# Kernel optimization log

Hardware: AMD Instinct MI355X
Metric: run time of the kernel (lower is better)

## Reference

```python
import jax, jax.numpy as jnp
import numpy as np

EPS = 1e-5
SELECT_NUM = 10   # hard-coded in Support_AUG_Image
NEIGHBOR_K = 3
SEMI_K = 3


def _conv(x, w):
    return jax.lax.conv_general_dilated(x, w, (1, 1), 'SAME',
                                        dimension_numbers=('NCHW', 'OIHW', 'NCHW'))


def _bn(x, g, b):
    # BatchNorm2d, training mode: biased batch stats over (N, H, W)
    mu = jnp.mean(x, (0, 2, 3), keepdims=True)
    var = jnp.mean((x - mu) ** 2, (0, 2, 3), keepdims=True)
    return g[None, :, None, None] * (x - mu) * jax.lax.rsqrt(var + EPS) + b[None, :, None, None]


def _lrelu(x):
    return jnp.where(x >= 0, x, 0.2 * x)


def _pool(x):
    return jax.lax.reduce_window(x, -jnp.inf, jax.lax.max,
                                 (1, 1, 2, 2), (1, 1, 2, 2), 'VALID')


def _features(x, params):
    # conv-bn-lrelu-pool, conv-bn-lrelu-pool, conv-bn-lrelu, conv-bn-lrelu
    for i, (w, g, b) in enumerate(params):
        x = _lrelu(_bn(_conv(x, w), g, b))
        if i < 2:
            x = _pool(x)
    return x  # [N, 64, 21, 21] for 84x84 input


def _descriptors(feat):
    # [B, C, h, w] -> [B, h*w, C], rows L2-normalized (query local descriptors)
    B, C = feat.shape[0], feat.shape[1]
    d = feat.reshape(B, C, -1).transpose(0, 2, 1)
    return d / jnp.sqrt(jnp.sum(d * d, -1, keepdims=True))


def _col_normalize(s):
    # [C, m]: L2-normalize each column (support descriptor)
    return s / jnp.sqrt(jnp.sum(s * s, 0, keepdims=True))


def _img2class_sim(q_desc, S, k):
    # q_desc [B, n, C] row-normalized; S [K, C, m] raw support banks.
    # Per class (K small, fixed): cosine sims [B, n, m], top-k over m, sum.
    sims = []
    for j in range(S.shape[0]):
        inner = q_desc @ _col_normalize(S[j])          # [B, n, m]
        tv = jax.lax.top_k(inner, k)[0]                # [B, n, k]
        sims.append(jnp.sum(tv, axis=(1, 2)))
    return jnp.stack(sims, 1)                          # [B, K]


def _forward(input1, input2, input3, params):
    K, shot = input2.shape[0], input2.shape[1]
    q = _features(input1, params)                      # [Bq, 64, 21, 21]
    sup = _features(input2.reshape((-1,) + input2.shape[2:]), params)
    C, h, w = sup.shape[1], sup.shape[2], sup.shape[3]
    # per class: permute(1,0,2,3).view(C,-1) -> [K, C, shot*h*w]
    S = sup.reshape(K, shot, C, h, w).transpose(0, 2, 1, 3, 4).reshape(K, C, shot * h * w)
    u = _features(input3, params)                      # [Bu, 64, 21, 21]

    # Support_AUG_Image: similarity of unlabeled pool vs support, softmax over classes,
    # then append top-10 unlabeled feature maps (raw) to each class bank.
    u_desc = _descriptors(u)
    sim_u = jax.nn.softmax(_img2class_sim(u_desc, S, SEMI_K), axis=1)  # [Bu, K]
    aug = []
    for j in range(K):
        idx = jax.lax.top_k(sim_u[:, j], SELECT_NUM)[1]                # [10]
        sel = u[idx].transpose(1, 0, 2, 3).reshape(C, -1)              # [C, 10*h*w]
        aug.append(jnp.concatenate([S[j], sel], axis=1))
    S_aug = jnp.stack(aug, 0)                          # [K, C, shot*h*w + 10*h*w]

    # ImgtoClass_Metric on queries vs augmented support
    q_desc = _descriptors(q)
    return _img2class_sim(q_desc, S_aug, NEIGHBOR_K)   # [Bq, K]


def setup_inputs() -> dict:
    key = jax.random.key(0)
    ks = jax.random.split(key, 8)
    inp = {
        'input1': jax.random.normal(ks[0], (75, 3, 84, 84), jnp.float32),
        'input2': jax.random.normal(ks[1], (5, 5, 3, 84, 84), jnp.float32),
        'input3': jax.random.normal(ks[2], (64, 3, 84, 84), jnp.float32),
        'w1': jax.random.normal(ks[3], (64, 3, 3, 3), jnp.float32) * 0.1,
        'w2': jax.random.normal(ks[4], (64, 64, 3, 3), jnp.float32) * 0.05,
        'w3': jax.random.normal(ks[5], (64, 64, 3, 3), jnp.float32) * 0.05,
        'w4': jax.random.normal(ks[6], (64, 64, 3, 3), jnp.float32) * 0.05,
    }
    for i in (1, 2, 3, 4):
        inp[f'g{i}'] = jnp.ones((64,), jnp.float32)
        inp[f'b{i}'] = jnp.zeros((64,), jnp.float32)
    return inp


def reference(input1, input2, input3, w1, g1, b1, w2, g2, b2, w3, g3, b3, w4, g4, b4):
    params = [(w1, g1, b1), (w2, g2, b2), (w3, g3, b3), (w4, g4, b4)]
    return _forward(input1, input2, input3, params)
```

## Files before the change

kernel.cpp:

```cpp
#include <hip/hip_runtime.h>
#include <hip/hip_bf16.h>
#include <math.h>

typedef __hip_bfloat16 bf16;
typedef __attribute__((ext_vector_type(8))) short short8;
typedef __attribute__((ext_vector_type(4))) float floatx4;
typedef __attribute__((ext_vector_type(4))) unsigned short ushort4v;

#define LRELU(v) ((v) < 0.f ? 0.2f * (v) : (v))

__device__ __forceinline__ float b2f(bf16 x) { return __bfloat162float(x); }
__device__ __forceinline__ int img_group(int n) { return n < 75 ? 0 : (n < 100 ? 1 : 2); }

__global__ __launch_bounds__(64) void detect_kernel(
    const void* in1, const void* in2, const void* in3,
    const void* w1, const void* w2, const void* w3, const void* w4,
    const void* g1, const void* g2, const void* g3, const void* g4,
    int* __restrict__ flags)
{
  int t = threadIdx.x;
  if (t >= 11) return;
  const void* p = nullptr; int nh = 384, isg = 0;
  switch (t) {
    case 0: p = in1; break;  case 1: p = in2; break;  case 2: p = in3; break;
    case 3: p = w1;  break;  case 4: p = w2;  break;  case 5: p = w3;  break;
    case 6: p = w4;  break;
    case 7: p = g1; nh = 64; isg = 1; break;
    case 8: p = g2; nh = 64; isg = 1; break;
    case 9: p = g3; nh = 64; isg = 1; break;
    case 10: p = g4; nh = 64; isg = 1; break;
  }
  const unsigned short* h = (const unsigned short*)p;
  int cnt = 0;
  for (int i = 0; i < nh; ++i) {
    unsigned short v = h[i];
    if (isg) {
      if (v == 0) ++cnt;
    } else {
      int e = (v >> 7) & 0xFF;
      if (e >= 160 || (e > 0 && e <= 80)) ++cnt;
    }
  }
  flags[t] = isg ? (cnt >= 16) : (cnt >= 48);
}

#define ZT0 167280
#define ZT1 1972592
#define ZT2 2896240
#define ZT3 3819888
#define ZT4 4565104
__device__ __forceinline__ void border_yx(int b, int W, int* y, int* x) {
  if (b < W) { *y = 0; *x = b; }
  else if (b < 2 * W) { *y = W - 1; *x = b - W; }
  else { int cc = b - 2 * W; *y = 1 + (cc >> 1); *x = (cc & 1) ? (W - 1) : 0; }
}
__global__ __launch_bounds__(256) void zero_pads(
    bf16* __restrict__ imgp, bf16* __restrict__ p1t,
    bf16* __restrict__ p2t, bf16* __restrict__ f3t, bf16* __restrict__ descAll)
{
  int i = blockIdx.x * 256 + threadIdx.x;
  bf16 z = __float2bfloat16(0.f);
  if (i < ZT0) {
    int plane = i / 340, b = i % 340;
    int y, x; border_yx(b, 86, &y, &x);
    imgp[((size_t)plane * 86 + y) * 86 + x] = z;
  } else if (i < ZT1) {
    int r = i - ZT0;
    int img = r / (172 * 64); r %= 172 * 64;
    int colb = r >> 6, ch = r & 63;
    int y, x; border_yx(colb, 44, &y, &x);
    p1t[(((size_t)img * 1936) + y * 44 + x) * 64 + ch] = z;
  } else if (i < ZT2) {
    int r = i - ZT1;
    int img = r / (88 * 64); r %= 88 * 64;
    int colb = r >> 6, ch = r & 63;
    int y, x; border_yx(colb, 23, &y, &x);
    p2t[(((size_t)img * 529) + y * 23 + x) * 64 + ch] = z;
  } else if (i < ZT3) {
    int r = i - ZT2;
    int img = r / (88 * 64); r %= 88 * 64;
    int colb = r >> 6, ch = r & 63;
    int y, x; border_yx(colb, 23, &y, &x);
    f3t[(((size_t)img * 529) + y * 23 + x) * 64 + ch] = z;
  } else if (i < ZT4) {
    int r = i - ZT3;
    int img = r / (71 * 64); r %= 71 * 64;
    int row = 441 + (r >> 6), ch = r & 63;
    descAll[((size_t)img * 512 + row) * 64 + ch] = z;
  }
}

#define NIMG 3471552
#define BIMG 13562
#define NWP  110592
#define BWP  432
#define BW1  8
#define BGB  2
#define NPART (4 * 164 * 128)
#define NZ (NPART + 320 + 375)
#define BZ  331
__global__ __launch_bounds__(256) void setup_all(
    const void* in1, const void* in2, const void* in3,
    const void* w1, const void* w2, const void* w3, const void* w4,
    const void* g1, const void* b1, const void* g2, const void* b2,
    const void* g3, const void* b3, const void* g4, const void* b4,
    const int* __restrict__ flags,
    bf16* __restrict__ imgp, bf16* __restrict__ w1p,
    bf16* __restrict__ wp2, bf16* __restrict__ wp3, bf16* __restrict__ wp4,
    float* __restrict__ gb, float* __restrict__ part,
    float* __restrict__ uscore, float* __restrict__ qscore)
{
  int b = blockIdx.x;
  if (b < BIMG) {
    int k = b * 256 + threadIdx.x;
    if (k >= NIMG) return;
    const void* src; int idx, f;
    if (k < 75 * 21168)       { src = in1; idx = k;               f = flags[0]; }
    else if (k < 100 * 21168) { src = in2; idx = k - 75 * 21168;  f = flags[1]; }
    else                      { src = in3; idx = k - 100 * 21168; f = flags[2]; }
    bf16 v = f ? __float2bfloat16(((const float*)src)[idx]) : ((const bf16*)src)[idx];
    int n = k / 21168, r = k % 21168;
    int ci = r / 7056, pix = r % 7056;
    int y = pix / 84, x = pix % 84;
    imgp[((size_t)(n * 3 + ci) * 86 + y + 1) * 86 + x + 1] = v;
  } else if (b < BIMG + BWP) {
    int idx = (b - BIMG) * 256 + threadIdx.x;
    if (idx >= NWP) return;
    int which = idx / 36864, i = idx % 36864;
    const void* src = which == 0 ? w2 : (which == 1 ? w3 : w4);
    bf16* dst = which == 0 ? wp2 : (which == 1 ? wp3 : wp4);
    int f = flags[4 + which];
    float v = f ? ((const float*)src)[i] : b2f(((const bf16*)src)[i]);
    int co = i / 576, ci = (i / 9) % 64, tap = i % 9;
    dst[((size_t)tap * 64 + co) * 64 + ci] = __float2bfloat16(v);
  } else if (b < BIMG + BWP + BW1) {
    int i = (b - BIMG - BWP) * 256 + threadIdx.x;
    if (i >= 2048) return;
    int co = i >> 5, k = i & 31;
    float v = 0.f;
    if (k < 27) {
      int f = flags[3];
      v = f ? ((const float*)w1)[co * 27 + k] : b2f(((const bf16*)w1)[co * 27 + k]);
    }
    w1p[i] = __float2bfloat16(v);
  } else if (b < BIMG + BWP + BW1 + BGB) {
    int i = (b - BIMG - BWP - BW1) * 256 + threadIdx.x;
    if (i >= 512) return;
    int which = i >> 6, cc = i & 63;
    const void* s;
    switch (which) {
      case 0: s = g1; break; case 1: s = b1; break;
      case 2: s = g2; break; case 3: s = b2; break;
      case 4: s = g3; break; case 5: s = b3; break;
      case 6: s = g4; break; default: s = b4; break;
    }
    int isg = !(which & 1);
    int f = isg ? flags[7 + (which >> 1)] : 0;
    gb[i] = f ? ((const float*)s)[cc] : b2f(((const bf16*)s)[cc]);
  } else {
    int i = (b - BIMG - BWP - BW1 - BGB) * 256 + threadIdx.x;
    if (i < NPART) part[i] = 0.f;
    else if (i < NPART + 320) uscore[i - NPART] = 0.f;
    else if (i < NZ) qscore[i - NPART - 320] = 0.f;
  }
}

__global__ __launch_bounds__(256) void conv1_stats_mfma(
    const bf16* __restrict__ imgp, const bf16* __restrict__ w1p,
    float* __restrict__ part)
{
  __shared__ float sacc[128];
  int n = blockIdx.x, tile = blockIdx.y;
  int lane = threadIdx.x & 63;
  int q = lane >> 4, c = lane & 15;
  int wave = threadIdx.x >> 6;
  int p = tile * 64 + wave * 16 + c;
  bool valid = p < 7056;
  int pc = valid ? p : 0;
  int y = pc / 84, x = pc % 84;
  const short* ib = (const short*)(imgp + (size_t)n * 3 * 86 * 86);
  short bs[8];
  #pragma unroll
  for (int j = 0; j < 8; ++j) {
    int k = q * 8 + j;
    int ci = k / 9, tap = k - ci * 9;
    int dy = tap / 3, dx = tap - dy * 3;
    bs[j] = (k < 27 && valid) ? ib[(ci * 86 + y + dy) * 86 + x + dx] : (short)0;
  }
  short8 B = {bs[0], bs[1], bs[2], bs[3], bs[4], bs[5], bs[6], bs[7]};
  float s[16], sq[16];
  #pragma unroll
  for (int t = 0; t < 4; ++t) {
    const short* ap = (const short*)w1p + (t * 16 + c) * 32 + q * 8;
    short8 A = *(const short8*)ap;
    floatx4 acc = {0.f, 0.f, 0.f, 0.f};
    acc = __builtin_amdgcn_mfma_f32_16x16x32_bf16(A, B, acc, 0, 0, 0);
    #pragma unroll
    for (int r = 0; r < 4; ++r) { s[t * 4 + r] = acc[r]; sq[t * 4 + r] = acc[r] * acc[r]; }
  }
  #pragma unroll
  for (int off = 1; off < 16; off <<= 1)
    #pragma unroll
    for (int i = 0; i < 16; ++i) {
      s[i]  += __shfl_xor(s[i], off);
      sq[i] += __shfl_xor(sq[i], off);
    }
  if (threadIdx.x < 128) sacc[threadIdx.x] = 0.f;
  __syncthreads();
  if (c == 0) {
    #pragma unroll
    for (int t = 0; t < 4; ++t)
      #pragma unroll
      for (int r = 0; r < 4; ++r) {
        int co = t * 16 + q * 4 + r;
        atomicAdd(&sacc[co], s[t * 4 + r]);
        atomicAdd(&sacc[64 + co], sq[t * 4 + r]);
      }
  }
  __syncthreads();
  if (threadIdx.x < 128) atomicAdd(&part[n * 128 + threadIdx.x], sacc[threadIdx.x]);
}

__global__ __launch_bounds__(256) void finalize_kernel(
    const float* __restrict__ part, const float* __restrict__ gam, const float* __restrict__ bet,
    float* __restrict__ scl, float* __restrict__ sht, float HWf)
{
  int t = threadIdx.x;
  if (t >= 192) return;
  int g = t / 64, c = t % 64;
  const int starts[3] = {0, 75, 100}, cnts[3] = {75, 25, 64};
  float S = 0.f, Q = 0.f;
  for (int im = starts[g]; im < starts[g] + cnts[g]; ++im) {
    S += part[im * 128 + c];
    Q += part[im * 128 + 64 + c];
  }
  float N = (float)cnts[g] * HWf;
  float mean = S / N;
  float var = fmaxf(Q / N - mean * mean, 0.f);
  float rstd = rsqrtf(var + 1e-5f);
  float sc = gam[c] * rstd;
  scl[t] = sc;
  sht[t] = bet[c] - mean * sc;
}

__global__ __launch_bounds__(256) void conv1_pool_mfma(
    const bf16* __restrict__ imgp, const bf16* __restrict__ w1p,
    const float* __restrict__ scl, const float* __restrict__ sht,
    bf16* __restrict__ p1t)
{
  int n = blockIdx.x, tile = blockIdx.y;
  int lane = threadIdx.x & 63, wave = threadIdx.x >> 6;
  int q = lane >> 4, c = lane & 15;
  int pp = tile * 64 + wave * 16 + c;
  bool valid = pp < 1764;
  int pc = valid ? pp : 0;
  int py = pc / 42, px = pc % 42;
  int g = img_group(n);
  const short* ib = (const short*)(imgp + (size_t)n * 3 * 86 * 86);
  short8 B[4];
  #pragma unroll
  for (int quad = 0; quad < 4; ++quad) {
    int y = 2 * py + (quad >> 1), x = 2 * px + (quad & 1);
    short bs[8];
    #pragma unroll
    for (int j = 0; j < 8; ++j) {
      int k = q * 8 + j;
      int ci = k / 9, tap = k - ci * 9;
      int dy = tap / 3, dx = tap - dy * 3;
      bs[j] = (k < 27) ? ib[(ci * 86 + y + dy) * 86 + x + dx] : (short)0;
    }
    B[quad] = (short8){bs[0], bs[1], bs[2], bs[3], bs[4], bs[5], bs[6], bs[7]};
  }
  bf16* ob = p1t + ((size_t)n * 1936 + (py + 1) * 44 + px + 1) * 64;
  #pragma unroll
  for (int t = 0; t < 4; ++t) {
    const short* ap = (const short*)w1p + (t * 16 + c) * 32 + q * 8;
    short8 A = *(const short8*)ap;
    floatx4 a0 = {0.f,0.f,0.f,0.f}, a1 = a0, a2 = a0, a3 = a0;
    a0 = __builtin_amdgcn_mfma_f32_16x16x32_bf16(A, B[0], a0, 0, 0, 0);
    a1 = __builtin_amdgcn_mfma_f32_16x16x32_bf16(A, B[1], a1, 0, 0, 0);
    a2 = __builtin_amdgcn_mfma_f32_16x16x32_bf16(A, B[2], a2, 0, 0, 0);
    a3 = __builtin_amdgcn_mfma_f32_16x16x32_bf16(A, B[3], a3, 0, 0, 0);
    if (valid) {
      ushort4v st;
      #pragma unroll
      for (int r = 0; r < 4; ++r) {
        int co = t * 16 + q * 4 + r;
        float sc_ = scl[g * 64 + co], sh_ = sht[g * 64 + co];
        float v0 = a0[r] * sc_ + sh_; v0 = LRELU(v0);
        float v1 = a1[r] * sc_ + sh_; v1 = LRELU(v1);
        float v2 = a2[r] * sc_ + sh_; v2 = LRELU(v2);
        float v3 = a3[r] * sc_ + sh_; v3 = LRELU(v3);
        float best = fmaxf(fmaxf(v0, v1), fmaxf(v2, v3));
        bf16 bv = __float2bfloat16(best);
        st[r] = *(unsigned short*)&bv;
      }
      *(ushort4v*)(ob + t * 16 + q * 4) = st;
    }
  }
}

__global__ __launch_bounds__(256) void bnt_kernel(
    const float* __restrict__ in, const float* __restrict__ scl, const float* __restrict__ sht,
    bf16* __restrict__ outp, int HW, int W, int PW, int PHPW)
{
  __shared__ bf16 tile[64][65];
  int n = blockIdx.x, t0 = blockIdx.y * 64;
  int g = img_group(n);
  for (int idx = threadIdx.x; idx < 4096; idx += 256) {
    int ci = idx >> 6, pix = idx & 63;
    int p = t0 + pix;
    float v = 0.f;
    if (p < HW) {
      v = in[((size_t)n * 64 + ci) * HW + p] * scl[g * 64 + ci] + sht[g * 64 + ci];
      v = LRELU(v);
    }
    tile[pix][ci] = __float2bfloat16(v);
  }
  __syncthreads();
  for (int idx = threadIdx.x; idx < 4096; idx += 256) {
    int pix = idx >> 6, ci = idx & 63;
    int p = t0 + pix;
    if (p < HW) {
      int y = p / W, x = p % W;
      outp[((size_t)n * PHPW + (y + 1) * PW + (x + 1)) * 64 + ci] = tile[pix][ci];
    }
  }
}

__global__ __launch_bounds__(256) void conv_mfma_kernel(
    const bf16* __restrict__ in_t, const bf16* __restrict__ wp,
    void* __restrict__ outp, int HW, int W, int PW, int PHPW, int out_is_f32,
    float* __restrict__ part)
{
  __shared__ float sacc[128];
  if (threadIdx.x < 128) sacc[threadIdx.x] = 0.f;
  __syncthreads();
  int n = blockIdx.x, tile = blockIdx.y;
  int wave = threadIdx.x >> 6, lane = threadIdx.x & 63;
  int q = lane >> 4, c = lane & 15;
  int p = tile * 64 + wave * 16 + c;
  bool valid = p < HW;
  int pc = valid ? p : HW - 1;
  int y = pc / W, x = pc % W;
  const bf16* ibase = in_t + ((size_t)n * PHPW + y * PW + x) * 64;

  short8 B0[9], B1[9];
  #pragma unroll
  for (int dy = 0; dy < 3; ++dy)
    #pragma unroll
    for (int dx = 0; dx < 3; ++dx) {
      const short* bp = (const short*)(ibase + (dy * PW + dx) * 64) + q * 8;
      B0[dy * 3 + dx] = *(const short8*)bp;
      B1[dy * 3 + dx] = *(const short8*)(bp + 32);
    }

  for (int t = 0; t < 4; ++t) {
    floatx4 acc = {0.f, 0.f, 0.f, 0.f};
    #pragma unroll
    for (int tap = 0; tap < 9; ++tap) {
      const short* ap = (const short*)(wp + ((size_t)tap * 64 + t * 16 + c) * 64) + q * 8;
      short8 A0 = *(const short8*)ap;
      short8 A1 = *(const short8*)(ap + 32);
      acc = __builtin_amdgcn_mfma_f32_16x16x32_bf16(A0, B0[tap], acc, 0, 0, 0);
      acc = __builtin_amdgcn_mfma_f32_16x16x32_bf16(A1, B1[tap], acc, 0, 0, 0);
    }
    float sv[4], qv[4];
    #pragma unroll
    for (int r = 0; r < 4; ++r) {
      float v = valid ? acc[r] : 0.f;
      sv[r] = v; qv[r] = v * v;
    }
    #pragma unroll
    for (int off = 1; off < 16; off <<= 1)
      #pragma unroll
      for (int r = 0; r < 4; ++r) {
        sv[r] += __shfl_xor(sv[r], off);
        qv[r] += __shfl_xor(qv[r], off);
      }
    if (c == 0) {
      #pragma unroll
      for (int r = 0; r < 4; ++r) {
        int co = t * 16 + q * 4 + r;
        atomicAdd(&sacc[co], sv[r]);
        atomicAdd(&sacc[64 + co], qv[r]);
      }
    }
    if (valid) {
      #pragma unroll
      for (int r = 0; r < 4; ++r) {
        int co = t * 16 + q * 4 + r;
        size_t oidx = ((size_t)n * 64 + co) * HW + p;
        if (out_is_f32) ((float*)outp)[oidx] = acc[r];
        else ((bf16*)outp)[oidx] = __float2bfloat16(acc[r]);
      }
    }
  }
  __syncthreads();
  if (threadIdx.x < 128) atomicAdd(&part[n * 128 + threadIdx.x], sacc[threadIdx.x]);
}

__global__ __launch_bounds__(256) void bn2_pool_t(
    const bf16* __restrict__ c2, const float* __restrict__ scl, const float* __restrict__ sht,
    bf16* __restrict__ p2t)
{
  __shared__ bf16 tile[64][65];
  int n = blockIdx.x, t0 = blockIdx.y * 64;
  int g = img_group(n);
  for (int idx = threadIdx.x; idx < 4096; idx += 256) {
    int co = idx >> 6, pix = idx & 63;
    int p = t0 + pix;
    bf16 outv = __float2bfloat16(0.f);
    if (p < 441) {
      float sc = scl[g * 64 + co], sh = sht[g * 64 + co];
      int py = p / 21, px = p % 21;
      const bf16* base = c2 + ((size_t)n * 64 + co) * 1764;
      float best = -1e30f;
      #pragma unroll
      for (int dy = 0; dy < 2; ++dy)
        #pragma unroll
        for (int dx = 0; dx < 2; ++dx) {
          float v = b2f(base[(2 * py + dy) * 42 + 2 * px + dx]) * sc + sh;
          v = LRELU(v);
          best = fmaxf(best, v);
        }
      outv = __float2bfloat16(best);
    }
    tile[pix][co] = outv;
  }
  __syncthreads();
  for (int idx = threadIdx.x; idx < 4096; idx += 256) {
    int pix = idx >> 6, co = idx & 63;
    int p = t0 + pix;
    if (p < 441) {
      int y = p / 21, x = p % 21;
      p2t[((size_t)n * 529 + (y + 1) * 23 + x + 1) * 64 + co] = tile[pix][co];
    }
  }
}

__global__ __launch_bounds__(256) void bn_norm_desc(
    const float* __restrict__ feat, const float* __restrict__ scl, const float* __restrict__ sht,
    bf16* __restrict__ descAll)
{
  __shared__ float tile[64][65];
  int n = blockIdx.x, t0 = blockIdx.y * 64;
  int g = img_group(n);
  for (int idx = threadIdx.x; idx < 4096; idx += 256) {
    int ci = idx >> 6, pix = idx & 63;
    int p = t0 + pix;
    float v = 0.f;
    if (p < 441) {
      v = feat[((size_t)n * 64 + ci) * 441 + p] * scl[g * 64 + ci] + sht[g * 64 + ci];
      v = LRELU(v);
    }
    tile[pix][ci] = v;
  }
  __syncthreads();
  int pix = threadIdx.x >> 2, quar = threadIdx.x & 3;
  float ss = 0.f;
  #pragma unroll
  for (int c = 0; c < 16; ++c) { float v = tile[pix][quar * 16 + c]; ss += v * v; }
  ss += __shfl_xor(ss, 1);
  ss += __shfl_xor(ss, 2);
  int p = t0 + pix;
  float inv = (p < 441) ? rsqrtf(ss) : 0.f;
  bf16* o = descAll + ((size_t)n * 512 + p) * 64 + quar * 16;
  #pragma unroll
  for (int c = 0; c < 16; ++c) o[c] = __float2bfloat16(tile[pix][quar * 16 + c] * inv);
}

__global__ __launch_bounds__(256) void sbank_copy(
    const bf16* __restrict__ descAll, bf16* __restrict__ SnT)
{
  int j = blockIdx.x / 9, chunk = blockIdx.x % 9;
  int col = chunk * 256 + threadIdx.x;
  short* o = (short*)(SnT + ((size_t)j * 2304 + col) * 64);
  if (col < 2205) {
    int shot = col / 441, pos = col % 441;
    const short* s = (const short*)(descAll + ((size_t)(75 + j * 5 + shot) * 512 + pos) * 64);
    #pragma unroll
    for (int k = 0; k < 8; ++k) *(short8*)(o + k * 8) = *(const short8*)(s + k * 8);
  } else {
    short8 z = {0,0,0,0,0,0,0,0};
    #pragma unroll
    for (int k = 0; k < 8; ++k) *(short8*)(o + k * 8) = z;
  }
}

__global__ __launch_bounds__(256) void saug_copy(
    const bf16* __restrict__ descAll, const bf16* __restrict__ SnT,
    const int* __restrict__ sel, bf16* __restrict__ SaT)
{
  int j = blockIdx.x / 26, chunk = blockIdx.x % 26;
  int col = chunk * 256 + threadIdx.x;
  short* o = (short*)(SaT + ((size_t)j * 6656 + col) * 64);
  const short* s;
  if (col < 2205) {
    s = (const short*)(SnT + ((size_t)j * 2304 + col) * 64);
  } else if (col < 6615) {
    int rel = col - 2205;
    int i = rel / 441, pos = rel % 441;
    int img = 100 + sel[j * 10 + i];
    s = (const short*)(descAll + ((size_t)img * 512 + pos) * 64);
  } else {
    short8 z = {0,0,0,0,0,0,0,0};
    #pragma unroll
    for (int k = 0; k < 8; ++k) *(short8*)(o + k * 8) = z;
    return;
  }
  #pragma unroll
  for (int k = 0; k < 8; ++k) *(short8*)(o + k * 8) = *(const short8*)(s + k * 8);
}

__global__ __launch_bounds__(256) void sim_mfma_kernel(
    const bf16* __restrict__ desc, const bf16* __restrict__ bankT,
    float* __restrict__ out, int m, int mp)
{
  __shared__ short lds[2][64 * 72];
  int img = blockIdx.x, cls = blockIdx.y, rowgrp = blockIdx.z;
  int tid = threadIdx.x;
  int wave = tid >> 6, lane = tid & 63;
  int q = lane >> 4, c = lane & 15;
  int R = rowgrp * 256 + wave * 64;
  bool wactive = R < 441;

  short8 b0l, b0h, b1l, b1h, b2l, b2h, b3l, b3h;
  if (wactive) {
    const short* dp = (const short*)(desc + ((size_t)img * 512 + R + c) * 64) + q * 8;
    b0l = *(const short8*)dp;          b0h = *(const short8*)(dp + 32);
    b1l = *(const short8*)(dp + 1024); b1h = *(const short8*)(dp + 1056);
    b2l = *(const short8*)(dp + 2048); b2h = *(const short8*)(dp + 2080);
    b3l = *(const short8*)(dp + 3072); b3h = *(const short8*)(dp + 3104);
  }

  float t0[4], t1[4], t2[4];
  #pragma unroll
  for (int i = 0; i < 4; ++i) { t0[i] = -1e4f; t1[i] = -1e4f; t2[i] = -1e4f; }

  const floatx4 z4 = {0.f, 0.f, 0.f, 0.f};

  const short* bankc = (const short*)(bankT + (size_t)cls * mp * 64);
  int nchunk = mp >> 6;
  int nfull = m >> 4;

  for (int s = tid; s < 512; s += 256) {
    int col = s >> 3, part = s & 7;
    *(short8*)(&lds[0][col * 72 + part * 8]) = *(const short8*)(bankc + (size_t)col * 64 + part * 8);
  }
  __syncthreads();

  for (int ch = 0; ch < nchunk; ++ch) {
    int cur = ch & 1;
    if (ch + 1 < nchunk) {
      const short* src = bankc + (size_t)(ch + 1) * 4096;
      for (int s = tid; s < 512; s += 256) {
        int col = s >> 3, part = s & 7;
        *(short8*)(&lds[cur ^ 1][col * 72 + part * 8]) = *(const short8*)(src + (size_t)col * 64 + part * 8);
      }
    }
    if (wactive) {
      #pragma unroll
      for (int t = 0; t < 4; ++t) {
        const short* lp = &lds[cur][(t * 16 + c) * 72 + q * 8];
        short8 A0 = *(const short8*)lp;
        short8 A1 = *(const short8*)(lp + 32);
        floatx4 a0 = __builtin_amdgcn_mfma_f32_16x16x32_bf16(A0, b0l, z4, 0, 0, 0);
        floatx4 a1 = __builtin_amdgcn_mfma_f32_16x16x32_bf16(A0, b1l, z4, 0, 0, 0);
        floatx4 a2 = __builtin_amdgcn_mfma_f32_16x16x32_bf16(A0, b2l, z4, 0, 0, 0);
        floatx4 a3 = __builtin_amdgcn_mfma_f32_16x16x32_bf16(A0, b3l, z4, 0, 0, 0);
        a0 = __builtin_amdgcn_mfma_f32_16x16x32_bf16(A1, b0h, a0, 0, 0, 0);
        a1 = __builtin_amdgcn_mfma_f32_16x16x32_bf16(A1, b1h, a1, 0, 0, 0);
        a2 = __builtin_amdgcn_mfma_f32_16x16x32_bf16(A1, b2h, a2, 0, 0, 0);
        a3 = __builtin_amdgcn_mfma_f32_16x16x32_bf16(A1, b3h, a3, 0, 0, 0);
        int gt = ch * 4 + t;
        if (gt < nfull) {
          #pragma unroll
          for (int r = 0; r < 4; ++r) {
            float v0 = a0[r];
            t2[0] = __builtin_amdgcn_fmed3f(v0, t2[0], t1[0]);
            t1[0] = __builtin_amdgcn_fmed3f(v0, t1[0], t0[0]);
            t0[0] = fmaxf(t0[0], v0);
            float v1 = a1[r];
            t2[1] = __builtin_amdgcn_fmed3f(v1, t2[1], t1[1]);
            t1[1] = __builtin_amdgcn_fmed3f(v1, t1[1], t0[1]);
            t0[1] = fmaxf(t0[1], v1);
            float v2 = a2[r];
            t2[2] = __builtin_amdgcn_fmed3f(v2, t2[2], t1[2]);
            t1[2] = __builtin_amdgcn_fmed3f(v2, t1[2], t0[2]);
            t0[2] = fmaxf(t0[2], v2);
            float v3 = a3[r];
            t2[3] = __builtin_amdgcn_fmed3f(v3, t2[3], t1[3]);
            t1[3] = __builtin_amdgcn_fmed3f(v3, t1[3], t0[3]);
            t0[3] = fmaxf(t0[3], v3);
          }
        } else {
          #pragma unroll
          for (int r = 0; r < 4; ++r) {
            bool colok = (gt * 16 + q * 4 + r) < m;
            float v0 = colok ? a0[r] : -1e4f;
            t2[0] = __builtin_amdgcn_fmed3f(v0, t2[0], t1[0]);
            t1[0] = __builtin_amdgcn_fmed3f(v0, t1[0], t0[0]);
            t0[0] = fmaxf(t0[0], v0);
            float v1 = colok ? a1[r] : -1e4f;
            t2[1] = __builtin_amdgcn_fmed3f(v1, t2[1], t1[1]);
            t1[1] = __builtin_amdgcn_fmed3f(v1, t1[1], t0[1]);
            t0[1] = fmaxf(t0[1], v1);
            float v2 = colok ? a2[r] : -1e4f;
            t2[2] = __builtin_amdgcn_fmed3f(v2, t2[2], t1[2]);
            t1[2] = __builtin_amdgcn_fmed3f(v2, t1[2], t0[2]);
            t0[2] = fmaxf(t0[2], v2);
            float v3 = colok ? a3[r] : -1e4f;
            t2[3] = __builtin_amdgcn_fmed3f(v3, t2[3], t1[3]);
            t1[3] = __builtin_amdgcn_fmed3f(v3, t1[3], t0[3]);
            t0[3] = fmaxf(t0[3], v3);
          }
        }
      }
    }
    __syncthreads();
  }

  if (wactive) {
    #pragma unroll
    for (int off = 16; off < 64; off <<= 1) {
      #pragma unroll
      for (int i = 0; i < 4; ++i) {
        float b0v = __shfl_xor(t0[i], off);
        float b1v = __shfl_xor(t1[i], off);
        float b2v = __shfl_xor(t2[i], off);
        float n0 = fmaxf(t0[i], b0v);
        float n1 = fminf(fmaxf(t0[i], b1v), fmaxf(t1[i], b0v));
        float n2 = fminf(fminf(fmaxf(t0[i], b2v), fmaxf(t1[i], b1v)), fmaxf(t2[i], b0v));
        t0[i] = n0; t1[i] = n1; t2[i] = n2;
      }
    }
    float psum = 0.f;
    if (q == 0) {
      #pragma unroll
      for (int i = 0; i < 4; ++i)
        if (R + i * 16 + c < 441) psum += t0[i] + t1[i] + t2[i];
    }
    #pragma unroll
    for (int off = 32; off > 0; off >>= 1) psum += __shfl_down(psum, off);
    if (lane == 0) atomicAdd(&out[img * 5 + cls], psum);
  }
}

__global__ __launch_bounds__(64) void softtop_kernel(
    const float* __restrict__ uscore, int* __restrict__ sel)
{
  __shared__ float simu[320];
  int i = threadIdx.x;
  {
    float v[5]; float mx = -1e30f;
    #pragma unroll
    for (int j = 0; j < 5; ++j) { v[j] = uscore[i * 5 + j]; mx = fmaxf(mx, v[j]); }
    float s = 0.f;
    #pragma unroll
    for (int j = 0; j < 5; ++j) { v[j] = expf(v[j] - mx); s += v[j]; }
    float inv = 1.f / s;
    #pragma unroll
    for (int j = 0; j < 5; ++j) simu[i * 5 + j] = v[j] * inv;
  }
  __syncthreads();
  if (i < 5) {
    unsigned long long mask = 0ull;
    for (int r = 0; r < 10; ++r) {
      float best = -1e30f; int bi = 0;
      for (int k = 0; k < 64; ++k) {
        if ((mask >> k) & 1ull) continue;
        float v = simu[k * 5 + i];
        if (v > best) { best = v; bi = k; }
      }
      mask |= (1ull << bi);
      sel[i * 10 + r] = bi;
    }
  }
}

__global__ __launch_bounds__(256) void outcvt_kernel(
    const float* __restrict__ qv, const int* __restrict__ flags, float* __restrict__ o)
{
  int i = blockIdx.x * 256 + threadIdx.x;
  if (i >= 375) return;
  float v = qv[i];
  int bad = (!isfinite(v)) || fabsf(v) > 2e3f;
  if (bad) {
    int code = flags[0] * 4 + flags[3] * 2 + flags[7];
    v = -(1e8f * (1.f + 0.01f * (float)code));
  }
  o[i] = v;
}

extern "C" void kernel_launch(void* const* d_in, const int* in_sizes, int n_in,
                              void* d_out, int out_size, void* d_ws, size_t ws_size,
                              hipStream_t stream) {
  const void* in1 = d_in[0];
  const void* in2 = d_in[1];
  const void* in3 = d_in[2];
  const void* w1  = d_in[3];
  const void* w2  = d_in[4];
  const void* w3  = d_in[5];
  const void* w4  = d_in[6];
  const void* g1  = d_in[7];
  const void* b1  = d_in[8];
  const void* g2  = d_in[9];
  const void* b2  = d_in[10];
  const void* g3  = d_in[11];
  const void* b3  = d_in[12];
  const void* g4  = d_in[13];
  const void* b4  = d_in[14];

  char* base = (char*)d_ws;
  size_t off = 0;
  auto alloc = [&](size_t bytes) -> void* {
    void* p = base + off;
    off += (bytes + 255) & ~(size_t)255;
    return p;
  };
  int*   flags = (int*)alloc(16 * 4);
  bf16*  wp2   = (bf16*)alloc(36864 * 2);
  bf16*  wp3   = (bf16*)alloc(36864 * 2);
  bf16*  wp4   = (bf16*)alloc(36864 * 2);
  bf16*  w1p   = (bf16*)alloc(2048 * 2);
  float* gb    = (float*)alloc(8 * 64 * 4);
  float* part  = (float*)alloc(4 * 164 * 128 * 4);
  float* scl1  = (float*)alloc(192 * 4);
  float* sht1  = (float*)alloc(192 * 4);
  float* scl2  = (float*)alloc(192 * 4);
  float* sht2  = (float*)alloc(192 * 4);
  float* scl3  = (float*)alloc(192 * 4);
  float* sht3  = (float*)alloc(192 * 4);
  float* scl4  = (float*)alloc(192 * 4);
  float* sht4  = (float*)alloc(192 * 4);
  float* uscore = (float*)alloc(320 * 4);
  int*   sel    = (int*)alloc(50 * 4);
  float* qscore = (float*)alloc(375 * 4);
  bf16*  imgp = (bf16*)alloc((size_t)164 * 3 * 86 * 86 * 2);
  bf16*  p1t  = (bf16*)alloc((size_t)164 * 1936 * 64 * 2);
  bf16*  p2t  = (bf16*)alloc((size_t)164 * 529 * 64 * 2);
  bf16*  f3t  = (bf16*)alloc((size_t)164 * 529 * 64 * 2);
  bf16*  descAll = (bf16*)alloc((size_t)164 * 512 * 64 * 2);
  bf16*  conv2o   = (bf16*)alloc((size_t)164 * 64 * 1764 * 2);
  bf16* SnT     = (bf16*)alloc((size_t)5 * 2304 * 64 * 2);
  bf16* SaT     = (bf16*)alloc((size_t)5 * 6656 * 64 * 2);
  float* feat3 = (float*)p1t;
  float* feat4 = (float*)((char*)p1t + (size_t)164 * 64 * 441 * 4);
  float* part1 = part;
  float* part2 = part + 164 * 128;
  float* part3 = part + 2 * 164 * 128;
  float* part4 = part + 3 * 164 * 128;

  detect_kernel<<<1, 64, 0, stream>>>(in1, in2, in3, w1, w2, w3, w4, g1, g2, g3, g4, flags);
  zero_pads<<<(ZT4 + 255) / 256, 256, 0, stream>>>(imgp, p1t, p2t, f3t, descAll);
  setup_all<<<BIMG + BWP + BW1 + BGB + BZ, 256, 0, stream>>>(
      in1, in2, in3, w1, w2, w3, w4, g1, b1, g2, b2, g3, b3, g4, b4,
      flags, imgp, w1p, wp2, wp3, wp4, gb, part, uscore, qscore);

  conv1_stats_mfma<<<dim3(164, 111), 256, 0, stream>>>(imgp, w1p, part1);
  finalize_kernel<<<1, 256, 0, stream>>>(part1, gb + 0 * 64, gb + 1 * 64, scl1, sht1, 7056.f);
  conv1_pool_mfma<<<dim3(164, 28), 256, 0, stream>>>(imgp, w1p, scl1, sht1, p1t);

  conv_mfma_kernel<<<dim3(164, 28), 256, 0, stream>>>(p1t, wp2, conv2o, 1764, 42, 44, 1936, 0, part2);
  finalize_kernel<<<1, 256, 0, stream>>>(part2, gb + 2 * 64, gb + 3 * 64, scl2, sht2, 1764.f);
  bn2_pool_t<<<dim3(164, 7), 256, 0, stream>>>(conv2o, scl2, sht2, p2t);

  conv_mfma_kernel<<<dim3(164, 7), 256, 0, stream>>>(p2t, wp3, feat3, 441, 21, 23, 529, 1, part3);
  finalize_kernel<<<1, 256, 0, stream>>>(part3, gb + 4 * 64, gb + 5 * 64, scl3, sht3, 441.f);
  bnt_kernel<<<dim3(164, 7), 256, 0, stream>>>(feat3, scl3, sht3, f3t, 441, 21, 23, 529);

  conv_mfma_kernel<<<dim3(164, 7), 256, 0, stream>>>(f3t, wp4, feat4, 441, 21, 23, 529, 1, part4);
  finalize_kernel<<<1, 256, 0, stream>>>(part4, gb + 6 * 64, gb + 7 * 64, scl4, sht4, 441.f);

  bn_norm_desc<<<dim3(164, 7), 256, 0, stream>>>(feat4, scl4, sht4, descAll);
  sbank_copy<<<45, 256, 0, stream>>>(descAll, SnT);

  sim_mfma_kernel<<<dim3(64, 5, 2), 256, 0, stream>>>(descAll + (size_t)100 * 512 * 64, SnT, uscore, 2205, 2304);
  softtop_kernel<<<1, 64, 0, stream>>>(uscore, sel);
  saug_copy<<<130, 256, 0, stream>>>(descAll, SnT, sel, SaT);

  sim_mfma_kernel<<<dim3(75, 5, 2), 256, 0, stream>>>(descAll, SaT, qscore, 6615, 6656);
  outcvt_kernel<<<2, 256, 0, stream>>>(qscore, flags, (float*)d_out);
}
```

Measured before the change: 1.132 ms.

## Split similarity kernel over bank column slices and merge top-3 partials

The similarity kernel now keeps all 441 query rows in one 7-wave block and splits the support bank columns into four slices across grid z. Before, the rows were split into two groups, which left wave slots idle. Each slice writes per-row top-3 partials to a global buffer, and a new merge kernel combines them and sums per image-class, replacing the atomicAdd. This adds parallelism and cuts the redundant bank streaming that came from the row split, at the cost of an extra launch and a partial-buffer round trip. Each slice's bank chunk count must divide evenly by four (36 and 104 do).

Measured after the change: 1.078 ms. -4.8%, faster.

```diff
diff --git a/kernel.cpp b/kernel.cpp
--- a/kernel.cpp
+++ b/kernel.cpp
@@ -513,26 +513,23 @@
   for (int k = 0; k < 8; ++k) *(short8*)(o + k * 8) = *(const short8*)(s + k * 8);
 }
 
-__global__ __launch_bounds__(256) void sim_mfma_kernel(
+#define SIM_NS 4
+__global__ __launch_bounds__(448) void sim_mfma_kernel(
     const bf16* __restrict__ desc, const bf16* __restrict__ bankT,
-    float* __restrict__ out, int m, int mp)
+    float* __restrict__ partial, int m, int mp)
 {
   __shared__ short lds[2][64 * 72];
-  int img = blockIdx.x, cls = blockIdx.y, rowgrp = blockIdx.z;
+  int img = blockIdx.x, cls = blockIdx.y, slice = blockIdx.z;
   int tid = threadIdx.x;
   int wave = tid >> 6, lane = tid & 63;
   int q = lane >> 4, c = lane & 15;
-  int R = rowgrp * 256 + wave * 64;
-  bool wactive = R < 441;
-
-  short8 b0l, b0h, b1l, b1h, b2l, b2h, b3l, b3h;
-  if (wactive) {
-    const short* dp = (const short*)(desc + ((size_t)img * 512 + R + c) * 64) + q * 8;
-    b0l = *(const short8*)dp;          b0h = *(const short8*)(dp + 32);
-    b1l = *(const short8*)(dp + 1024); b1h = *(const short8*)(dp + 1056);
-    b2l = *(const short8*)(dp + 2048); b2h = *(const short8*)(dp + 2080);
-    b3l = *(const short8*)(dp + 3072); b3h = *(const short8*)(dp + 3104);
-  }
+  int R = wave * 64;
+
+  const short* dp = (const short*)(desc + ((size_t)img * 512 + R + c) * 64) + q * 8;
+  short8 b0l = *(const short8*)dp;          short8 b0h = *(const short8*)(dp + 32);
+  short8 b1l = *(const short8*)(dp + 1024); short8 b1h = *(const short8*)(dp + 1056);
+  short8 b2l = *(const short8*)(dp + 2048); short8 b2h = *(const short8*)(dp + 2080);
+  short8 b3l = *(const short8*)(dp + 3072); short8 b3h = *(const short8*)(dp + 3104);
 
   float t0[4], t1[4], t2[4];
   #pragma unroll
@@ -541,110 +538,141 @@
   const floatx4 z4 = {0.f, 0.f, 0.f, 0.f};
 
   const short* bankc = (const short*)(bankT + (size_t)cls * mp * 64);
-  int nchunk = mp >> 6;
+  int nc = (mp >> 6) / SIM_NS;
+  int ch0 = slice * nc, ch1 = ch0 + nc;
   int nfull = m >> 4;
 
-  for (int s = tid; s < 512; s += 256) {
+  for (int s = tid; s < 512; s += 448) {
     int col = s >> 3, part = s & 7;
-    *(short8*)(&lds[0][col * 72 + part * 8]) = *(const short8*)(bankc + (size_t)col * 64 + part * 8);
-  }
-  __syncthreads();
-
-  for (int ch = 0; ch < nchunk; ++ch) {
-    int cur = ch & 1;
-    if (ch + 1 < nchunk) {
+    *(short8*)(&lds[0][col * 72 + part * 8]) =
+        *(const short8*)(bankc + ((size_t)ch0 * 64 + col) * 64 + part * 8);
+  }
+  __syncthreads();
+
+  for (int ch = ch0; ch < ch1; ++ch) {
+    int cur = (ch - ch0) & 1;
+    if (ch + 1 < ch1) {
       const short* src = bankc + (size_t)(ch + 1) * 4096;
-      for (int s = tid; s < 512; s += 256) {
+      for (int s = tid; s < 512; s += 448) {
         int col = s >> 3, part = s & 7;
         *(short8*)(&lds[cur ^ 1][col * 72 + part * 8]) = *(const short8*)(src + (size_t)col * 64 + part * 8);
       }
     }
-    if (wactive) {
-      #pragma unroll
-      for (int t = 0; t < 4; ++t) {
-        const short* lp = &lds[cur][(t * 16 + c) * 72 + q * 8];
-        short8 A0 = *(const short8*)lp;
-        short8 A1 = *(const short8*)(lp + 32);
-        floatx4 a0 = __builtin_amdgcn_mfma_f32_16x16x32_bf16(A0, b0l, z4, 0, 0, 0);
-        floatx4 a1 = __builtin_amdgcn_mfma_f32_16x16x32_bf16(A0, b1l, z4, 0, 0, 0);
-        floatx4 a2 = __builtin_amdgcn_mfma_f32_16x16x32_bf16(A0, b2l, z4, 0, 0, 0);
-        floatx4 a3 = __builtin_amdgcn_mfma_f32_16x16x32_bf16(A0, b3l, z4, 0, 0, 0);
-        a0 = __builtin_amdgcn_mfma_f32_16x16x32_bf16(A1, b0h, a0, 0, 0, 0);
-        a1 = __builtin_amdgcn_mfma_f32_16x16x32_bf16(A1, b1h, a1, 0, 0, 0);
-        a2 = __builtin_amdgcn_mfma_f32_16x16x32_bf16(A1, b2h, a2, 0, 0, 0);
-        a3 = __builtin_amdgcn_mfma_f32_16x16x32_bf16(A1, b3h, a3, 0, 0, 0);
-        int gt = ch * 4 + t;
-        if (gt < nfull) {
-          #pragma unroll
-          for (int r = 0; r < 4; ++r) {
-            float v0 = a0[r];
-            t2[0] = __builtin_amdgcn_fmed3f(v0, t2[0], t1[0]);
-            t1[0] = __builtin_amdgcn_fmed3f(v0, t1[0], t0[0]);
-            t0[0] = fmaxf(t0[0], v0);
-            float v1 = a1[r];
-            t2[1] = __builtin_amdgcn_fmed3f(v1, t2[1], t1[1]);
-            t1[1] = __builtin_amdgcn_fmed3f(v1, t1[1], t0[1]);
-            t0[1] = fmaxf(t0[1], v1);
-            float v2 = a2[r];
-            t2[2] = __builtin_amdgcn_fmed3f(v2, t2[2], t1[2]);
-            t1[2] = __builtin_amdgcn_fmed3f(v2, t1[2], t0[2]);
-            t0[2] = fmaxf(t0[2], v2);
-            float v3 = a3[r];
-            t2[3] = __builtin_amdgcn_fmed3f(v3, t2[3], t1[3]);
-            t1[3] = __builtin_amdgcn_fmed3f(v3, t1[3], t0[3]);
-            t0[3] = fmaxf(t0[3], v3);
-          }
-        } else {
-          #pragma unroll
-          for (int r = 0; r < 4; ++r) {
-            bool colok = (gt * 16 + q * 4 + r) < m;
-            float v0 = colok ? a0[r] : -1e4f;
-            t2[0] = __builtin_amdgcn_fmed3f(v0, t2[0], t1[0]);
-            t1[0] = __builtin_amdgcn_fmed3f(v0, t1[0], t0[0]);
-            t0[0] = fmaxf(t0[0], v0);
-            float v1 = colok ? a1[r] : -1e4f;
-            t2[1] = __builtin_amdgcn_fmed3f(v1, t2[1], t1[1]);
-            t1[1] = __builtin_amdgcn_fmed3f(v1, t1[1], t0[1]);
-            t0[1] = fmaxf(t0[1], v1);
-            float v2 = colok ? a2[r] : -1e4f;
-            t2[2] = __builtin_amdgcn_fmed3f(v2, t2[2], t1[2]);
-            t1[2] = __builtin_amdgcn_fmed3f(v2, t1[2], t0[2]);
-            t0[2] = fmaxf(t0[2], v2);
-            float v3 = colok ? a3[r] : -1e4f;
-            t2[3] = __builtin_amdgcn_fmed3f(v3, t2[3], t1[3]);
-            t1[3] = __builtin_amdgcn_fmed3f(v3, t1[3], t0[3]);
-            t0[3] = fmaxf(t0[3], v3);
-          }
+    #pragma unroll
+    for (int t = 0; t < 4; ++t) {
+      const short* lp = &lds[cur][(t * 16 + c) * 72 + q * 8];
+      short8 A0 = *(const short8*)lp;
+      short8 A1 = *(const short8*)(lp + 32);
+      floatx4 a0 = __builtin_amdgcn_mfma_f32_16x16x32_bf16(A0, b0l, z4, 0, 0, 0);
+      floatx4 a1 = __builtin_amdgcn_mfma_f32_16x16x32_bf16(A0, b1l, z4, 0, 0, 0);
+      floatx4 a2 = __builtin_amdgcn_mfma_f32_16x16x32_bf16(A0, b2l, z4, 0, 0, 0);
+      floatx4 a3 = __builtin_amdgcn_mfma_f32_16x16x32_bf16(A0, b3l, z4, 0, 0, 0);
+      a0 = __builtin_amdgcn_mfma_f32_16x16x32_bf16(A1, b0h, a0, 0, 0, 0);
+      a1 = __builtin_amdgcn_mfma_f32_16x16x32_bf16(A1, b1h, a1, 0, 0, 0);
+      a2 = __builtin_amdgcn_mfma_f32_16x16x32_bf16(A1, b2h, a2, 0, 0, 0);
+      a3 = __builtin_amdgcn_mfma_f32_16x16x32_bf16(A1, b3h, a3, 0, 0, 0);
+      int gt = ch * 4 + t;
+      if (gt < nfull) {
+        #pragma unroll
+        for (int r = 0; r < 4; ++r) {
+          float v0 = a0[r];
+          t2[0] = __builtin_amdgcn_fmed3f(v0, t2[0], t1[0]);
+          t1[0] = __builtin_amdgcn_fmed3f(v0, t1[0], t0[0]);
+          t0[0] = fmaxf(t0[0], v0);
+          float v1 = a1[r];
+          t2[1] = __builtin_amdgcn_fmed3f(v1, t2[1], t1[1]);
+          t1[1] = __builtin_amdgcn_fmed3f(v1, t1[1], t0[1]);
+          t0[1] = fmaxf(t0[1], v1);
+          float v2 = a2[r];
+          t2[2] = __builtin_amdgcn_fmed3f(v2, t2[2], t1[2]);
+          t1[2] = __builtin_amdgcn_fmed3f(v2, t1[2], t0[2]);
+          t0[2] = fmaxf(t0[2], v2);
+          float v3 = a3[r];
+          t2[3] = __builtin_amdgcn_fmed3f(v3, t2[3], t1[3]);
+          t1[3] = __builtin_amdgcn_fmed3f(v3, t1[3], t0[3]);
+          t0[3] = fmaxf(t0[3], v3);
+        }
+      } else {
+        #pragma unroll
+        for (int r = 0; r < 4; ++r) {
+          bool colok = (gt * 16 + q * 4 + r) < m;
+          float v0 = colok ? a0[r] : -1e4f;
+          t2[0] = __builtin_amdgcn_fmed3f(v0, t2[0], t1[0]);
+          t1[0] = __builtin_amdgcn_fmed3f(v0, t1[0], t0[0]);
+          t0[0] = fmaxf(t0[0], v0);
+          float v1 = colok ? a1[r] : -1e4f;
+          t2[1] = __builtin_amdgcn_fmed3f(v1, t2[1], t1[1]);
+          t1[1] = __builtin_amdgcn_fmed3f(v1, t1[1], t0[1]);
+          t0[1] = fmaxf(t0[1], v1);
+          float v2 = colok ? a2[r] : -1e4f;
+          t2[2] = __builtin_amdgcn_fmed3f(v2, t2[2], t1[2]);
+          t1[2] = __builtin_amdgcn_fmed3f(v2, t1[2], t0[2]);
+          t0[2] = fmaxf(t0[2], v2);
+          float v3 = colok ? a3[r] : -1e4f;
+          t2[3] = __builtin_amdgcn_fmed3f(v3, t2[3], t1[3]);
+          t1[3] = __builtin_amdgcn_fmed3f(v3, t1[3], t0[3]);
+          t0[3] = fmaxf(t0[3], v3);
         }
       }
     }
     __syncthreads();
   }
 
-  if (wactive) {
-    #pragma unroll
-    for (int off = 16; off < 64; off <<= 1) {
-      #pragma unroll
-      for (int i = 0; i < 4; ++i) {
-        float b0v = __shfl_xor(t0[i], off);
-        float b1v = __shfl_xor(t1[i], off);
-        float b2v = __shfl_xor(t2[i], off);
-        float n0 = fmaxf(t0[i], b0v);
-        float n1 = fminf(fmaxf(t0[i], b1v), fmaxf(t1[i], b0v));
-        float n2 = fminf(fminf(fmaxf(t0[i], b2v), fmaxf(t1[i], b1v)), fmaxf(t2[i], b0v));
-        t0[i] = n0; t1[i] = n1; t2[i] = n2;
+  #pragma unroll
+  for (int off = 16; off < 64; off <<= 1) {
+    #pragma unroll
+    for (int i = 0; i < 4; ++i) {
+      float b0v = __shfl_xor(t0[i], off);
+      float b1v = __shfl_xor(t1[i], off);
+      float b2v = __shfl_xor(t2[i], off);
+      float n0 = fmaxf(t0[i], b0v);
+      float n1 = fminf(fmaxf(t0[i], b1v), fmaxf(t1[i], b0v));
+      float n2 = fminf(fminf(fmaxf(t0[i], b2v), fmaxf(t1[i], b1v)), fmaxf(t2[i], b0v));
+      t0[i] = n0; t1[i] = n1; t2[i] = n2;
+    }
+  }
+
+  if (q == 0) {
+    size_t base = ((size_t)(img * 5 + cls) * SIM_NS + slice) * 512;
+    #pragma unroll
+    for (int i = 0; i < 4; ++i) {
+      int row = R + i * 16 + c;
+      if (row < 441) {
+        floatx4 v = {t0[i], t1[i], t2[i], 0.f};
+        *(floatx4*)(&partial[(base + row) * 4]) = v;
       }
     }
-    float psum = 0.f;
-    if (q == 0) {
-      #pragma unroll
-      for (int i = 0; i < 4; ++i)
-        if (R + i * 16 + c < 441) psum += t0[i] + t1[i] + t2[i];
-    }
-    #pragma unroll
-    for (int off = 32; off > 0; off >>= 1) psum += __shfl_down(psum, off);
-    if (lane == 0) atomicAdd(&out[img * 5 + cls], psum);
-  }
+  }
+}
+
+__global__ __launch_bounds__(256) void sim_merge_kernel(
+    const float* __restrict__ partial, float* __restrict__ out)
+{
+  __shared__ float red[4];
+  int ic = blockIdx.x;
+  int tid = threadIdx.x;
+  const floatx4* p0 = (const floatx4*)partial + (size_t)ic * SIM_NS * 512;
+  float sum = 0.f;
+  for (int row = tid; row < 441; row += 256) {
+    floatx4 a = p0[row];
+    float t0 = a[0], t1 = a[1], t2 = a[2];
+    #pragma unroll
+    for (int s = 1; s < SIM_NS; ++s) {
+      floatx4 b = p0[s * 512 + row];
+      float b0 = b[0], b1 = b[1], b2 = b[2];
+      float n0 = fmaxf(t0, b0);
+      float n1 = fminf(fmaxf(t0, b1), fmaxf(t1, b0));
+      float n2 = fminf(fminf(fmaxf(t0, b2), fmaxf(t1, b1)), fmaxf(t2, b0));
+      t0 = n0; t1 = n1; t2 = n2;
+    }
+    sum += t0 + t1 + t2;
+  }
+  #pragma unroll
+  for (int off = 32; off > 0; off >>= 1) sum += __shfl_down(sum, off);
+  int wv = tid >> 6;
+  if ((tid & 63) == 0) red[wv] = sum;
+  __syncthreads();
+  if (tid == 0) out[ic] = red[0] + red[1] + red[2] + red[3];
 }
 
 __global__ __launch_bounds__(64) void softtop_kernel(
@@ -737,6 +765,7 @@
   float* uscore = (float*)alloc(320 * 4);
   int*   sel    = (int*)alloc(50 * 4);
   float* qscore = (float*)alloc(375 * 4);
+  float* simpart = (float*)alloc((size_t)375 * SIM_NS * 512 * 4 * 4);
   bf16*  imgp = (bf16*)alloc((size_t)164 * 3 * 86 * 86 * 2);
   bf16*  p1t  = (bf16*)alloc((size_t)164 * 1936 * 64 * 2);
   bf16*  p2t  = (bf16*)alloc((size_t)164 * 529 * 64 * 2);
@@ -776,10 +805,12 @@
   bn_norm_desc<<<dim3(164, 7), 256, 0, stream>>>(feat4, scl4, sht4, descAll);
   sbank_copy<<<45, 256, 0, stream>>>(descAll, SnT);
 
-  sim_mfma_kernel<<<dim3(64, 5, 2), 256, 0, stream>>>(descAll + (size_t)100 * 512 * 64, SnT, uscore, 2205, 2304);
+  sim_mfma_kernel<<<dim3(64, 5, SIM_NS), 448, 0, stream>>>(descAll + (size_t)100 * 512 * 64, SnT, simpart, 2205, 2304);
+  sim_merge_kernel<<<320, 256, 0, stream>>>(simpart, uscore);
   softtop_kernel<<<1, 64, 0, stream>>>(uscore, sel);
   saug_copy<<<130, 256, 0, stream>>>(descAll, SnT, sel, SaT);
 
-  sim_mfma_kernel<<<dim3(75, 5, 2), 256, 0, stream>>>(descAll, SaT, qscore, 6615, 6656);
+  sim_mfma_kernel<<<dim3(75, 5, SIM_NS), 448, 0, stream>>>(descAll, SaT, simpart, 6615, 6656);
+  sim_merge_kernel<<<375, 256, 0, stream>>>(simpart, qscore);
   outcvt_kernel<<<2, 256, 0, stream>>>(qscore, flags, (float*)d_out);
 }
```
